# Optimization experiments

Measured on AMD Instinct MI355X. Metric: run time of the kernel, lower is better.

## Reference

```python
import jax, jax.numpy as jnp
import numpy as np

B, N, NUM_CLASSES = 2, 131072, 2
SCORE_THR, IOU_THR, OUT_NUM = 0.05, 0.7, 2000
NEG = -1e9  # sentinel for suppressed / below-threshold scores


def _decode(deltas, anchors):
    h = anchors[..., 2] - anchors[..., 0]
    w = anchors[..., 3] - anchors[..., 1]
    cy = (anchors[..., 2] + anchors[..., 0]) * 0.5
    cx = (anchors[..., 3] + anchors[..., 1]) * 0.5
    d = deltas * jnp.array([0.1, 0.1, 0.2, 0.2], dtype=deltas.dtype)
    cy = cy + d[..., 0] * h
    cx = cx + d[..., 1] * w
    h = h * jnp.exp(d[..., 2])
    w = w * jnp.exp(d[..., 3])
    return jnp.stack([cy - h * 0.5, cx - w * 0.5, cy + h * 0.5, cx + w * 0.5], axis=-1)


def _iou(box, boxes):
    # box [4] vs boxes [N,4] -> [N]
    y1 = jnp.maximum(box[0], boxes[:, 0])
    x1 = jnp.maximum(box[1], boxes[:, 1])
    y2 = jnp.minimum(box[2], boxes[:, 2])
    x2 = jnp.minimum(box[3], boxes[:, 3])
    inter = jnp.maximum(y2 - y1, 0.0) * jnp.maximum(x2 - x1, 0.0)
    a1 = (box[2] - box[0]) * (box[3] - box[1])
    a2 = (boxes[:, 2] - boxes[:, 0]) * (boxes[:, 3] - boxes[:, 1])
    return inter / (a1 + a2 - inter + 1e-8)


def _nms_single(boxes, scores, logits):
    # greedy NMS (= tf.image.non_max_suppression), then gather + pad_to_fixed_size
    live0 = jnp.where(scores > SCORE_THR, scores, NEG)

    def step(live, _):
        best = jnp.argmax(live)
        ok = live[best] > NEG * 0.5
        iou = _iou(boxes[best], boxes)
        live = jnp.where((iou > IOU_THR) & ok, NEG, live)
        live = live.at[best].set(NEG)
        return live, (best.astype(jnp.int32), ok.astype(boxes.dtype))

    _, (sel, valid) = jax.lax.scan(step, live0, None, length=OUT_NUM)
    vb = valid[:, None]  # [OUT_NUM,1] pad tag: 1 for real rows, 0 for padding
    out_boxes = boxes[sel] * vb
    out_scores = scores[sel][:, None] * vb
    out_logits = logits[sel] * vb
    return (jnp.concatenate([out_boxes, vb], axis=-1),
            jnp.concatenate([out_scores, vb], axis=-1),
            jnp.concatenate([out_logits, vb], axis=-1))


def _forward(deltas, class_logits, anchors):
    probs = jax.nn.softmax(class_logits, axis=-1)
    fg_scores = jnp.max(probs[..., 1:], axis=-1)  # [B,N]
    boxes = _decode(deltas, anchors)              # [B,N,4]
    return jax.vmap(_nms_single)(boxes, fg_scores, class_logits)


def setup_inputs() -> dict:
    key = jax.random.key(0)
    k1, k2, k3, k4, k5, k6 = jax.random.split(key, 6)
    deltas = jax.random.normal(k1, (B, N, 4), jnp.float32) * 0.5
    class_logits = jax.random.normal(k2, (B, N, NUM_CLASSES), jnp.float32)
    cy = jax.random.uniform(k3, (B, N), minval=0.0, maxval=800.0)
    cx = jax.random.uniform(k4, (B, N), minval=0.0, maxval=800.0)
    h = jax.random.uniform(k5, (B, N), minval=16.0, maxval=256.0)
    w = jax.random.uniform(k6, (B, N), minval=16.0, maxval=256.0)
    anchors = jnp.stack([cy - h * 0.5, cx - w * 0.5, cy + h * 0.5, cx + w * 0.5], axis=-1)
    return {"deltas": deltas, "class_logits": class_logits, "anchors": anchors}


def reference(deltas, class_logits, anchors):
    return _forward(deltas, class_logits, anchors)
```

## Files before the change

kernel.cpp:

```cpp
#include <hip/hip_runtime.h>
#include <stdint.h>
#include <stddef.h>

#define BATCH 2
#define NELEM 131072
#define OUT_NUM 2000
#define KCAP 32
#define PREWIN 16384
#define KPRE_W (PREWIN / 64)

__device__ __forceinline__ float exp32cr(float x) { return (float)exp((double)x); }

__device__ __forceinline__ bool iou_gt(float by1, float bx1, float by2, float bx2,
                                       float cy1, float cx1, float cy2, float cx2) {
    float y1 = fmaxf(by1, cy1), x1 = fmaxf(bx1, cx1);
    float y2 = fminf(by2, cy2), x2 = fminf(bx2, cx2);
    float ih = __fsub_rn(y2, y1), iw = __fsub_rn(x2, x1);
    if (ih <= 0.0f || iw <= 0.0f) return false;
    float inter = __fmul_rn(ih, iw);
    float a1 = __fmul_rn(__fsub_rn(by2, by1), __fsub_rn(bx2, bx1));
    float a2 = __fmul_rn(__fsub_rn(cy2, cy1), __fsub_rn(cx2, cx1));
    float den = __fadd_rn(__fsub_rn(__fadd_rn(a1, a2), inter), 1e-8f);
    float rhs = __fmul_rn(0.7f, den);
    if (inter > __fmul_rn(rhs, 1.0001f)) return true;
    if (inter < __fmul_rn(rhs, 0.9999f)) return false;
    return __fdiv_rn(inter, den) > 0.7f;
}
__device__ __forceinline__ bool iou_gt4(float4 a, float4 c) {
    return iou_gt(a.x, a.y, a.z, a.w, c.x, c.y, c.z, c.w);
}

__device__ __forceinline__ bool maybe4(float4 A, float4 C) {
    float dy = fabsf((A.x + A.z) - (C.x + C.z));
    float dx = fabsf((A.y + A.w) - (C.y + C.w));
    float hs = (A.z - A.x) + (C.z - C.x);
    float ws = (A.w - A.y) + (C.w - C.y);
    return (dy < 0.19f * hs) && (dx < 0.19f * ws);
}

__device__ __forceinline__ void decode_f(const float* __restrict__ deltas,
                                         const float* __restrict__ anchors,
                                         size_t gi, float* bx) {
    float a0 = anchors[4 * gi], a1 = anchors[4 * gi + 1];
    float a2 = anchors[4 * gi + 2], a3 = anchors[4 * gi + 3];
    float h = __fsub_rn(a2, a0), w = __fsub_rn(a3, a1);
    float cy = __fmul_rn(__fadd_rn(a2, a0), 0.5f);
    float cx = __fmul_rn(__fadd_rn(a3, a1), 0.5f);
    float d0 = __fmul_rn(deltas[4 * gi], 0.1f);
    float d1 = __fmul_rn(deltas[4 * gi + 1], 0.1f);
    float d2 = __fmul_rn(deltas[4 * gi + 2], 0.2f);
    float d3 = __fmul_rn(deltas[4 * gi + 3], 0.2f);
    cy = __fadd_rn(cy, __fmul_rn(d0, h));
    cx = __fadd_rn(cx, __fmul_rn(d1, w));
    h = __fmul_rn(h, exp32cr(d2));
    w = __fmul_rn(w, exp32cr(d3));
    bx[0] = __fsub_rn(cy, __fmul_rn(h, 0.5f));
    bx[1] = __fsub_rn(cx, __fmul_rn(w, 0.5f));
    bx[2] = __fadd_rn(cy, __fmul_rn(h, 0.5f));
    bx[3] = __fadd_rn(cx, __fmul_rn(w, 0.5f));
}

__device__ __forceinline__ float score_f(const float* __restrict__ logits, size_t gi) {
    float l0 = logits[2 * gi], l1 = logits[2 * gi + 1];
    float m = fmaxf(l0, l1);
    float e0 = exp32cr(__fsub_rn(l0, m));
    float e1 = exp32cr(__fsub_rn(l1, m));
    return __fdiv_rn(e1, __fadd_rn(e0, e1));
}

__global__ __launch_bounds__(256) void prep_kernel(
    const float* __restrict__ logits, uint64_t* __restrict__ keys,
    uint32_t* __restrict__ flag, uint32_t* __restrict__ state) {
    int i = blockIdx.x * 256 + threadIdx.x;
    if (i == 0) *flag = 0;
    if (i < 32) state[i] = 0;
    if (i >= BATCH * NELEM) return;
    float s = score_f(logits, (size_t)i);
    uint32_t idx = (uint32_t)(i & (NELEM - 1));
    uint64_t key = 0;
    if (s > 0.05f)
        key = ((uint64_t)__float_as_uint(s) << 17) | ((~idx) & 0x1FFFFu);
    keys[i] = key;
}

__global__ __launch_bounds__(1024) void bitonic_local_sort4(uint64_t* __restrict__ keys) {
    __shared__ uint64_t sh[4096];
    const int t = threadIdx.x;
    const size_t base = (size_t)blockIdx.x * 4096;
    for (int e = t; e < 4096; e += 1024) sh[e] = keys[base + e];
    __syncthreads();
    const int gb = (int)(base & (NELEM - 1));
    for (int k = 2; k <= 4096; k <<= 1) {
        for (int j = k >> 1; j >= 1; j >>= 1) {
            for (int pp = t; pp < 2048; pp += 1024) {
                int a = ((pp & ~(j - 1)) << 1) | (pp & (j - 1));
                bool ddd = (((gb + a) & k) == 0);
                uint64_t x = sh[a], y = sh[a + j];
                bool sw = ddd ? (x < y) : (x > y);
                if (sw) { sh[a] = y; sh[a + j] = x; }
            }
            __syncthreads();
        }
    }
    for (int e = t; e < 4096; e += 1024) keys[base + e] = sh[e];
}

__global__ __launch_bounds__(256) void bitonic_global_pass(uint64_t* __restrict__ keys,
                                                           int k, int j) {
    int tid = blockIdx.x * blockDim.x + threadIdx.x;
    const int half = NELEM / 2;
    int b = tid / half;
    int tt = tid - b * half;
    int a = ((tt & ~(j - 1)) << 1) | (tt & (j - 1));
    uint64_t* kb = keys + (size_t)b * NELEM;
    bool ddd = ((a & k) == 0);
    uint64_t x = kb[a], y = kb[a + j];
    bool sw = ddd ? (x < y) : (x > y);
    if (sw) { kb[a] = y; kb[a + j] = x; }
}

__global__ __launch_bounds__(256) void bitonic_global_fused2(uint64_t* __restrict__ keys,
                                                             int k, int j) {
    int tid = blockIdx.x * 256 + threadIdx.x;
    const int q = NELEM / 4;
    int b = tid / q;
    int tt = tid - b * q;
    int jh = j >> 1;
    int x = ((tt & ~(jh - 1)) << 2) | (tt & (jh - 1));
    uint64_t* kb = keys + (size_t)b * NELEM;
    bool ddd = ((x & k) == 0);
    uint64_t e0 = kb[x], e1 = kb[x + jh], e2 = kb[x + j], e3 = kb[x + j + jh];
    uint64_t tmp;
#define CMPEX(A, B) { bool sw = ddd ? (A < B) : (A > B); if (sw) { tmp = A; A = B; B = tmp; } }
    CMPEX(e0, e2) CMPEX(e1, e3)
    CMPEX(e0, e1) CMPEX(e2, e3)
#undef CMPEX
    kb[x] = e0; kb[x + jh] = e1; kb[x + j] = e2; kb[x + j + jh] = e3;
}

__global__ __launch_bounds__(1024) void bitonic_local_merge8(uint64_t* __restrict__ keys,
                                                             int k) {
    __shared__ uint64_t sh[8192];
    const int t = threadIdx.x;
    const size_t base = (size_t)blockIdx.x * 8192;
    for (int e = t; e < 8192; e += 1024) sh[e] = keys[base + e];
    __syncthreads();
    const bool ddd = (((int)(base & (NELEM - 1)) & k) == 0);
    for (int j = 4096; j >= 1; j >>= 1) {
        for (int pp = t; pp < 4096; pp += 1024) {
            int a = ((pp & ~(j - 1)) << 1) | (pp & (j - 1));
            uint64_t x = sh[a], y = sh[a + j];
            bool sw = ddd ? (x < y) : (x > y);
            if (sw) { sh[a] = y; sh[a + j] = x; }
        }
        __syncthreads();
    }
    for (int e = t; e < 8192; e += 1024) keys[base + e] = sh[e];
}

__global__ __launch_bounds__(256) void sort_check(const uint64_t* __restrict__ keys,
                                                  uint32_t* __restrict__ flag) {
    int i = blockIdx.x * 256 + threadIdx.x;
    if (i >= BATCH * NELEM) return;
    uint32_t q = (uint32_t)i & (NELEM - 1);
    if (q != NELEM - 1) {
        if (keys[i] < keys[i + 1]) atomicOr(flag, 1u);
    }
}

__global__ __launch_bounds__(256) void records_kernel(
    const uint64_t* __restrict__ keys, const float* __restrict__ deltas,
    const float* __restrict__ anchors, const float* __restrict__ logits,
    float* __restrict__ records, uint32_t* __restrict__ kcount, int M) {
    int g = blockIdx.x * 256 + threadIdx.x;
    if (g >= BATCH * M) return;
    kcount[g] = 0;
    int b = g / M, r = g - b * M;
    uint64_t key = keys[(size_t)b * NELEM + r];
    float4 r0, r1;
    if (key != 0) {
        uint32_t idx = (uint32_t)((~key) & 0x1FFFFu);
        size_t gi = (size_t)b * NELEM + idx;
        float bx[4];
        decode_f(deltas, anchors, gi, bx);
        r0 = make_float4(bx[0], bx[1], bx[2], bx[3]);
        r1 = make_float4(score_f(logits, gi), logits[2 * gi], logits[2 * gi + 1], 1.0f);
    } else {
        r0 = make_float4(0.f, 0.f, 0.f, 0.f);
        r1 = make_float4(0.f, 0.f, 0.f, 0.f);
    }
    float4* rp = (float4*)records;
    rp[(size_t)g * 2] = r0;
    rp[(size_t)g * 2 + 1] = r1;
}

__global__ __launch_bounds__(64) void mask_kernel(const float* __restrict__ records,
                                                  uint64_t* __restrict__ masks,
                                                  uint32_t* __restrict__ kcount,
                                                  uint16_t* __restrict__ klist, int M) {
    int ti = blockIdx.x, tj = blockIdx.y, b = blockIdx.z;
    if (tj > ti) return;
    int t = threadIdx.x;
    __shared__ float4 jb[64];
    __shared__ int jv[64];
    const float4* rp = (const float4*)records;
    {
        float4 rj  = rp[((size_t)b * M + (size_t)tj * 64 + t) * 2];
        float4 rj1 = rp[((size_t)b * M + (size_t)tj * 64 + t) * 2 + 1];
        jb[t] = rj;
        jv[t] = (rj1.w != 0.f);
    }
    const int i = ti * 64 + t;
    float4 ri  = rp[((size_t)b * M + i) * 2];
    float4 ri1 = rp[((size_t)b * M + i) * 2 + 1];
    bool iv = (ri1.w != 0.f);
    __syncthreads();
    uint64_t word = 0;
    if (iv) {
        for (int jj = 0; jj < 64; ++jj) {
            bool earlier = (tj < ti) || (jj < t);
            if (earlier && jv[jj] && maybe4(jb[jj], ri) && iou_gt4(jb[jj], ri)) {
                word |= 1ull << jj;
                uint32_t slot = atomicAdd(&kcount[(size_t)b * M + i], 1u);
                if (slot < KCAP)
                    klist[((size_t)b * M + i) * KCAP + slot] = (uint16_t)(tj * 64 + jj);
            }
        }
    }
    masks[((size_t)b * M + i) * (size_t)(M >> 6) + tj] = word;
}

__global__ void nms_walk(
    const float* __restrict__ records, const uint64_t* __restrict__ masks,
    const uint32_t* __restrict__ kcount, const uint16_t* __restrict__ klist,
    float4* __restrict__ accbox, uint32_t* __restrict__ state,
    float* __restrict__ out, int M) {
    const int b = blockIdx.x;
    const int t = threadIdx.x;
    const int Wm = M >> 6;
    const int NC = M >> 8;
    const uint64_t* mb = masks + (size_t)b * M * (size_t)Wm;
    const float4* rp = (const float4*)records + (size_t)b * M * 2;

    __shared__ uint64_t accset[128];
    __shared__ uint64_t bwLDS[256][4];
    __shared__ uint8_t kf[256];
    __shared__ float4 recLDS[512];
    __shared__ uint32_t s_state[16];

    for (int w = t; w < 128; w += blockDim.x) accset[w] = 0;
    __syncthreads();

    int n_acc = 0, done = 0;
    for (int ci = 0; ci < NC && !done; ++ci) {
        const int p = ci << 8;
        const int pw = ci << 2;
        if (t < 256) {
            const int gi = p + t;
            uint32_t cnt = kcount[(size_t)b * M + gi];
            uint64_t rq0 = 0, rq1 = 0, rq2 = 0, rq3 = 0;
            bool kill = false;
            if (cnt <= KCAP) {
                const uint16_t* lp = klist + ((size_t)b * M + gi) * KCAP;
                for (uint32_t u = 0; u < cnt; ++u) {
                    int j = lp[u];
                    if (j < p) {
                        if ((accset[j >> 6] >> (j & 63)) & 1) kill = true;
                    } else {
                        int d = j - p;
                        uint64_t bit = 1ull << (d & 63);
                        switch (d >> 6) {
                            case 0: rq0 |= bit; break;
                            case 1: rq1 |= bit; break;
                            case 2: rq2 |= bit; break;
                            default: rq3 |= bit; break;
                        }
                    }
                }
            } else {
                const uint64_t* row = mb + (size_t)gi * Wm;
                uint64_t o = 0;
                for (int w = 0; w < pw; ++w) o |= row[w] & accset[w];
                kill = (o != 0);
                rq0 = row[pw]; rq1 = row[pw + 1];
                rq2 = row[pw + 2]; rq3 = row[pw + 3];
            }
            kf[t] = kill ? 1 : 0;
            bwLDS[t][0] = rq0; bwLDS[t][1] = rq1;
            bwLDS[t][2] = rq2; bwLDS[t][3] = rq3;
        } else if (t < 512) {
            int i0 = t - 256;
            recLDS[i0] = rp[(size_t)p * 2 + i0];
            recLDS[i0 + 256] = rp[(size_t)p * 2 + i0 + 256];
        }
        __syncthreads();

        if (t < 64) {
            const int l = t;
            uint64_t b00 = bwLDS[l][0], b01 = bwLDS[l][1], b02 = bwLDS[l][2], b03 = bwLDS[l][3];
            uint64_t b10 = bwLDS[64 + l][0], b11 = bwLDS[64 + l][1], b12 = bwLDS[64 + l][2], b13 = bwLDS[64 + l][3];
            uint64_t b20 = bwLDS[128 + l][0], b21 = bwLDS[128 + l][1], b22 = bwLDS[128 + l][2], b23 = bwLDS[128 + l][3];
            uint64_t b30 = bwLDS[192 + l][0], b31 = bwLDS[192 + l][1], b32 = bwLDS[192 + l][2], b33 = bwLDS[192 + l][3];
            uint64_t vm0 = __ballot(recLDS[2 * l + 1].w != 0.f);
            uint64_t vm1 = __ballot(recLDS[2 * (64 + l) + 1].w != 0.f);
            uint64_t vm2 = __ballot(recLDS[2 * (128 + l) + 1].w != 0.f);
            uint64_t vm3 = __ballot(recLDS[2 * (192 + l) + 1].w != 0.f);
            uint64_t k0 = __ballot(kf[l] != 0);
            uint64_t k1 = __ballot(kf[64 + l] != 0);
            uint64_t k2 = __ballot(kf[128 + l] != 0);
            uint64_t k3 = __ballot(kf[192 + l] != 0);
            uint64_t e0m = __ballot((b00 | b01 | b02 | b03) == 0);
            uint64_t e1m = __ballot((b10 | b11 | b12 | b13) == 0);
            uint64_t e2m = __ballot((b20 | b21 | b22 | b23) == 0);
            uint64_t e3m = __ballot((b30 | b31 | b32 | b33) == 0);
            if (t == 0) {
                uint64_t t0 = vm0 & ~k0, t1 = vm1 & ~k1, t2 = vm2 & ~k2, t3 = vm3 & ~k3;
                uint64_t a0 = t0 & e0m, a1 = t1 & e1m, a2 = t2 & e2m, a3 = t3 & e3m;
                uint64_t c0 = t0 & ~e0m, c1 = t1 & ~e1m, c2 = t2 & ~e2m, c3 = t3 & ~e3m;
#define RESOLVE(cq, aq, base) \
    while (cq) { int cb = __builtin_ctzll(cq); cq &= cq - 1; \
        int idx = (base) + cb; \
        uint64_t w0 = bwLDS[idx][0], w1 = bwLDS[idx][1]; \
        uint64_t w2 = bwLDS[idx][2], w3 = bwLDS[idx][3]; \
        if (!((w0 & a0) | (w1 & a1) | (w2 & a2) | (w3 & a3))) aq |= (1ull << cb); }
                RESOLVE(c0, a0, 0)
                RESOLVE(c1, a1, 64)
                RESOLVE(c2, a2, 128)
                RESOLVE(c3, a3, 192)
#undef RESOLVE
                int n = n_acc;
                int dn = ((vm0 & vm1 & vm2 & vm3) != ~0ull) ? 1 : 0;
                int tot = (int)(__popcll(a0) + __popcll(a1) + __popcll(a2) + __popcll(a3));
                int rem = OUT_NUM - n;
                if (tot >= rem) {
                    int keep = rem;
#define TRUNC(w) { int pc = (int)__popcll(w); \
    if (keep >= pc) keep -= pc; \
    else { while ((int)__popcll(w) > keep) w &= ~(1ull << (63 - __builtin_clzll(w))); keep = 0; } }
                    TRUNC(a0) TRUNC(a1) TRUNC(a2) TRUNC(a3)
#undef TRUNC
                    n = OUT_NUM; dn = 1;
                } else {
                    n += tot;
                }
                s_state[0] = (uint32_t)n_acc;
                s_state[1] = (uint32_t)n;
                s_state[2] = (uint32_t)dn;
                s_state[3] = (uint32_t)a0; s_state[4] = (uint32_t)(a0 >> 32);
                s_state[5] = (uint32_t)a1; s_state[6] = (uint32_t)(a1 >> 32);
                s_state[7] = (uint32_t)a2; s_state[8] = (uint32_t)(a2 >> 32);
                s_state[9] = (uint32_t)a3; s_state[10] = (uint32_t)(a3 >> 32);
                accset[pw] = a0; accset[pw + 1] = a1;
                accset[pw + 2] = a2; accset[pw + 3] = a3;
            }
        }
        __syncthreads();
        int r0 = (int)s_state[0];
        n_acc = (int)s_state[1];
        done = (int)s_state[2];
        uint64_t amA = ((uint64_t)s_state[4] << 32) | s_state[3];
        uint64_t amB = ((uint64_t)s_state[6] << 32) | s_state[5];
        uint64_t amC = ((uint64_t)s_state[8] << 32) | s_state[7];
        uint64_t amD = ((uint64_t)s_state[10] << 32) | s_state[9];

        if (t < 256) {
            int q = t >> 6, ll = t & 63;
            uint64_t amq = q == 0 ? amA : q == 1 ? amB : q == 2 ? amC : amD;
            if ((amq >> ll) & 1) {
                int base = r0;
                if (q > 0) base += (int)__popcll(amA);
                if (q > 1) base += (int)__popcll(amB);
                if (q > 2) base += (int)__popcll(amC);
                int row = base + (int)__popcll(amq & ((1ull << ll) - 1ull));
                float4 cb = recLDS[t * 2], cm = recLDS[t * 2 + 1];
                accbox[(size_t)b * OUT_NUM + row] = cb;
                float* ob = out + ((size_t)b * OUT_NUM + row) * 5;
                ob[0] = cb.x; ob[1] = cb.y; ob[2] = cb.z; ob[3] = cb.w; ob[4] = 1.0f;
                float* os = out + (size_t)BATCH * OUT_NUM * 5 +
                            ((size_t)b * OUT_NUM + row) * 2;
                os[0] = cm.x; os[1] = 1.0f;
                float* ol = out + (size_t)BATCH * OUT_NUM * 7 +
                            ((size_t)b * OUT_NUM + row) * 3;
                ol[0] = cm.y; ol[1] = cm.z; ol[2] = 1.0f;
            }
        }
        __syncthreads();
    }
    if (t == 0) {
        state[b * 16] = (uint32_t)n_acc;
        state[b * 16 + 1] = (uint32_t)done;
    }
}

__global__ __launch_bounds__(1024) void prekill_kernel(
    const uint64_t* __restrict__ keys, const float* __restrict__ deltas,
    const float* __restrict__ anchors, const float4* __restrict__ accbox,
    const uint32_t* __restrict__ state, uint64_t* __restrict__ kpre, int Mend) {
    const int blk = blockIdx.x, b = blockIdx.y;
    const int t = threadIdx.x;
    const int c = t & 63, g = t >> 6;
    const int n1 = (int)state[b * 16];
    __shared__ float4 aF[OUT_NUM];
    __shared__ float4 jb[64];
    __shared__ uint8_t kfl[64];
    for (int r = t; r < n1; r += 1024) aF[r] = accbox[(size_t)b * OUT_NUM + r];
    if (t < 64) {
        kfl[t] = 0;
        int j = Mend + blk * 64 + t;
        uint64_t key = keys[(size_t)b * NELEM + j];
        float4 bx4 = make_float4(0.f, 0.f, 0.f, 0.f);
        if (key != 0) {
            uint32_t idx = (uint32_t)((~key) & 0x1FFFFu);
            size_t gi = (size_t)b * NELEM + idx;
            float bx[4];
            decode_f(deltas, anchors, gi, bx);
            bx4 = make_float4(bx[0], bx[1], bx[2], bx[3]);
        }
        jb[t] = bx4;
    }
    __syncthreads();
    float4 cb = jb[c];
    float csy = cb.x + cb.z, csx = cb.y + cb.w;
    float ch19 = 0.19f * (cb.z - cb.x), cw19 = 0.19f * (cb.w - cb.y);
    bool k = false;
    for (int a = g; a < n1; a += 16) {
        float4 af = aF[a];
        float asy = af.x + af.z, asx = af.y + af.w;
        float ah19 = 0.19f * (af.z - af.x), aw19 = 0.19f * (af.w - af.y);
        if (fabsf(asy - csy) < ah19 + ch19 && fabsf(asx - csx) < aw19 + cw19) {
            if (iou_gt4(af, cb)) { k = true; break; }
        }
    }
    if (k) kfl[c] = 1;
    __syncthreads();
    if (t < 64) {
        uint64_t w = __ballot(kfl[t] != 0);
        if (t == 0) kpre[(size_t)b * KPRE_W + blk] = w;
    }
}

__global__ __launch_bounds__(512) void nms_tail(
    const uint64_t* __restrict__ keys, const float* __restrict__ deltas,
    const float* __restrict__ logits, const float* __restrict__ anchors,
    const float4* __restrict__ accbox, const uint32_t* __restrict__ state,
    const uint64_t* __restrict__ kpre, float* __restrict__ out,
    int Mend, int hasPre) {
    const int b = blockIdx.x;
    const int t = threadIdx.x;
    const int l = t & 63;

    __shared__ float4 aF4[OUT_NUM];
    __shared__ float4 aS4[OUT_NUM];
    __shared__ float4 cbox[256], cmeta[256];
    __shared__ uint32_t transW[256][8];
    __shared__ uint8_t kf2[512];
    __shared__ uint64_t kpreLDS[4];
    __shared__ uint32_t s_state[16];

    if (t == 0) {
        s_state[0] = state[b * 16];
        s_state[1] = state[b * 16 + 1];
    }
    __syncthreads();
    int n_acc = (int)s_state[0];
    int done = (int)s_state[1];
    const int tailStart = n_acc;
    for (int r = t; r < n_acc; r += 512) {
        float4 ab = accbox[(size_t)b * OUT_NUM + r];
        aF4[r] = ab;
        aS4[r] = make_float4(ab.x + ab.z, ab.y + ab.w, ab.z - ab.x, ab.w - ab.y);
    }
    __syncthreads();

    for (int p = Mend; p < NELEM && !done; p += 256) {
        const bool inwin = hasPre && (p < Mend + PREWIN);
        for (int i = t; i < 2048; i += 512) ((uint32_t*)transW)[i] = 0;
        if (t < 256) {
            uint64_t key = keys[(size_t)b * NELEM + p + t];
            float4 bx4 = make_float4(0.f, 0.f, 0.f, 0.f);
            float4 mt = make_float4(0.f, 0.f, 0.f, 0.f);
            if (key != 0) {
                uint32_t idx = (uint32_t)((~key) & 0x1FFFFu);
                size_t gi = (size_t)b * NELEM + idx;
                float bx[4];
                decode_f(deltas, anchors, gi, bx);
                bx4 = make_float4(bx[0], bx[1], bx[2], bx[3]);
                mt = make_float4(score_f(logits, gi), logits[2 * gi],
                                 logits[2 * gi + 1], 1.0f);
            }
            cbox[t] = bx4; cmeta[t] = mt;
        }
        if (t < 4)
            kpreLDS[t] = inwin ? kpre[(size_t)b * KPRE_W + ((p - Mend) >> 6) + t] : 0ull;
        __syncthreads();

        {
            const int c = t & 255, g = t >> 8;
            float4 cb = cbox[c];
            bool pkc = inwin && ((kpreLDS[c >> 6] >> (c & 63)) & 1);
            bool valid = (cmeta[c].w != 0.f) && !pkc;
            float csy = cb.x + cb.z, csx = cb.y + cb.w;
            float chh = cb.z - cb.x, cww = cb.w - cb.y;
            bool k = false;
            int aStart = inwin ? tailStart : 0;
            if (valid) {
                for (int a = aStart + g; a < n_acc; a += 2) {
                    float4 as = aS4[a];
                    if (fabsf(as.x - csy) < 0.19f * (as.z + chh) &&
                        fabsf(as.y - csx) < 0.19f * (as.w + cww)) {
                        if (iou_gt4(aF4[a], cb)) { k = true; break; }
                    }
                }
            }
            kf2[t] = k ? 1 : 0;
        }
        __syncthreads();

        for (int pid = t; pid < 256 * 256; pid += 512) {
            int c0 = pid >> 8, c1 = pid & 255;
            if (c1 > c0 && cmeta[c0].w != 0.f && cmeta[c1].w != 0.f) {
                bool d0 = (inwin && ((kpreLDS[c0 >> 6] >> (c0 & 63)) & 1)) ||
                          kf2[c0] || kf2[256 + c0];
                bool d1 = (inwin && ((kpreLDS[c1 >> 6] >> (c1 & 63)) & 1)) ||
                          kf2[c1] || kf2[256 + c1];
                if (!d0 && !d1 && maybe4(cbox[c0], cbox[c1]) &&
                    iou_gt4(cbox[c0], cbox[c1]))
                    atomicOr(&transW[c1][c0 >> 5], 1u << (c0 & 31));
            }
        }
        __syncthreads();

        if (t < 64) {
            uint64_t bw00, bw01, bw02, bw03, bw10, bw11, bw12, bw13;
            uint64_t bw20, bw21, bw22, bw23, bw30, bw31, bw32, bw33;
            bw00 = ((uint64_t)transW[l][1] << 32) | transW[l][0];
            bw01 = ((uint64_t)transW[l][3] << 32) | transW[l][2];
            bw02 = ((uint64_t)transW[l][5] << 32) | transW[l][4];
            bw03 = ((uint64_t)transW[l][7] << 32) | transW[l][6];
            bw10 = ((uint64_t)transW[64 + l][1] << 32) | transW[64 + l][0];
            bw11 = ((uint64_t)transW[64 + l][3] << 32) | transW[64 + l][2];
            bw12 = ((uint64_t)transW[64 + l][5] << 32) | transW[64 + l][4];
            bw13 = ((uint64_t)transW[64 + l][7] << 32) | transW[64 + l][6];
            bw20 = ((uint64_t)transW[128 + l][1] << 32) | transW[128 + l][0];
            bw21 = ((uint64_t)transW[128 + l][3] << 32) | transW[128 + l][2];
            bw22 = ((uint64_t)transW[128 + l][5] << 32) | transW[128 + l][4];
            bw23 = ((uint64_t)transW[128 + l][7] << 32) | transW[128 + l][6];
            bw30 = ((uint64_t)transW[192 + l][1] << 32) | transW[192 + l][0];
            bw31 = ((uint64_t)transW[192 + l][3] << 32) | transW[192 + l][2];
            bw32 = ((uint64_t)transW[192 + l][5] << 32) | transW[192 + l][4];
            bw33 = ((uint64_t)transW[192 + l][7] << 32) | transW[192 + l][6];
            uint64_t vm0 = __ballot(cmeta[l].w != 0.f);
            uint64_t vm1 = __ballot(cmeta[64 + l].w != 0.f);
            uint64_t vm2 = __ballot(cmeta[128 + l].w != 0.f);
            uint64_t vm3 = __ballot(cmeta[192 + l].w != 0.f);
            uint64_t k0 = kpreLDS[0] | __ballot((kf2[l] | kf2[256 + l]) != 0);
            uint64_t k1 = kpreLDS[1] | __ballot((kf2[64 + l] | kf2[320 + l]) != 0);
            uint64_t k2 = kpreLDS[2] | __ballot((kf2[128 + l] | kf2[384 + l]) != 0);
            uint64_t k3 = kpreLDS[3] | __ballot((kf2[192 + l] | kf2[448 + l]) != 0);
            uint64_t t0 = vm0 & ~k0, t1 = vm1 & ~k1, t2 = vm2 & ~k2, t3 = vm3 & ~k3;
            uint64_t am0 = 0, am1 = 0, am2 = 0, am3 = 0;
            int n = n_acc;
            int dn = ((vm0 & vm1 & vm2 & vm3) != ~0ull);
            while (t0 | t1 | t2 | t3) {
                int qb; uint64_t w;
                if (t0)      { qb = 0; w = t0; }
                else if (t1) { qb = 1; w = t1; }
                else if (t2) { qb = 2; w = t2; }
                else         { qb = 3; w = t3; }
                int lb = __builtin_ctzll(w);
                uint64_t bit = 1ull << lb;
                if (qb == 0) { am0 |= bit; t0 &= ~bit; }
                else if (qb == 1) { am1 |= bit; t1 &= ~bit; }
                else if (qb == 2) { am2 |= bit; t2 &= ~bit; }
                else { am3 |= bit; t3 &= ~bit; }
                ++n;
                if (n == OUT_NUM) { dn = 1; break; }
                uint64_t s0 = qb == 0 ? bw00 : qb == 1 ? bw01 : qb == 2 ? bw02 : bw03;
                uint64_t s1 = qb == 0 ? bw10 : qb == 1 ? bw11 : qb == 2 ? bw12 : bw13;
                uint64_t s2 = qb == 0 ? bw20 : qb == 1 ? bw21 : qb == 2 ? bw22 : bw23;
                uint64_t s3 = qb == 0 ? bw30 : qb == 1 ? bw31 : qb == 2 ? bw32 : bw33;
                t0 &= ~__ballot(((s0 >> lb) & 1) != 0);
                t1 &= ~__ballot(((s1 >> lb) & 1) != 0);
                t2 &= ~__ballot(((s2 >> lb) & 1) != 0);
                t3 &= ~__ballot(((s3 >> lb) & 1) != 0);
            }
            if (t == 0) {
                s_state[0] = (uint32_t)n_acc;
                s_state[1] = (uint32_t)n;
                s_state[2] = (uint32_t)dn;
                s_state[3] = (uint32_t)am0; s_state[4] = (uint32_t)(am0 >> 32);
                s_state[5] = (uint32_t)am1; s_state[6] = (uint32_t)(am1 >> 32);
                s_state[7] = (uint32_t)am2; s_state[8] = (uint32_t)(am2 >> 32);
                s_state[9] = (uint32_t)am3; s_state[10] = (uint32_t)(am3 >> 32);
            }
        }
        __syncthreads();
        int r0 = (int)s_state[0];
        n_acc = (int)s_state[1];
        done = (int)s_state[2];
        uint64_t amA = ((uint64_t)s_state[4] << 32) | s_state[3];
        uint64_t amB = ((uint64_t)s_state[6] << 32) | s_state[5];
        uint64_t amC = ((uint64_t)s_state[8] << 32) | s_state[7];
        uint64_t amD = ((uint64_t)s_state[10] << 32) | s_state[9];

        if (t < 256) {
            int q = t >> 6, ll = t & 63;
            uint64_t amq = q == 0 ? amA : q == 1 ? amB : q == 2 ? amC : amD;
            if ((amq >> ll) & 1) {
                int base = r0;
                if (q > 0) base += (int)__popcll(amA);
                if (q > 1) base += (int)__popcll(amB);
                if (q > 2) base += (int)__popcll(amC);
                int row = base + (int)__popcll(amq & ((1ull << ll) - 1ull));
                float4 cb = cbox[t];
                float4 cm = cmeta[t];
                aF4[row] = cb;
                aS4[row] = make_float4(cb.x + cb.z, cb.y + cb.w,
                                       cb.z - cb.x, cb.w - cb.y);
                float* ob = out + ((size_t)b * OUT_NUM + row) * 5;
                ob[0] = cb.x; ob[1] = cb.y; ob[2] = cb.z; ob[3] = cb.w; ob[4] = 1.0f;
                float* os = out + (size_t)BATCH * OUT_NUM * 5 +
                            ((size_t)b * OUT_NUM + row) * 2;
                os[0] = cm.x; os[1] = 1.0f;
                float* ol = out + (size_t)BATCH * OUT_NUM * 7 +
                            ((size_t)b * OUT_NUM + row) * 3;
                ol[0] = cm.y; ol[1] = cm.z; ol[2] = 1.0f;
            }
        }
        __syncthreads();
    }

    for (int r = n_acc + t; r < OUT_NUM; r += 512) {
        float* ob = out + ((size_t)b * OUT_NUM + r) * 5;
        ob[0] = 0.f; ob[1] = 0.f; ob[2] = 0.f; ob[3] = 0.f; ob[4] = 0.f;
        float* os = out + (size_t)BATCH * OUT_NUM * 5 + ((size_t)b * OUT_NUM + r) * 2;
        os[0] = 0.f; os[1] = 0.f;
        float* ol = out + (size_t)BATCH * OUT_NUM * 7 + ((size_t)b * OUT_NUM + r) * 3;
        ol[0] = 0.f; ol[1] = 0.f; ol[2] = 0.f;
    }
    if (t == 0 && n_acc < OUT_NUM) out[0] = 2.0e5f;
}

__global__ void canary_kernel(const uint32_t* __restrict__ flag, float* __restrict__ out,
                              int code) {
    if (code) { out[0] = 3.0e5f; return; }
    if (*flag) out[0] = 1.0e5f;
}

extern "C" void kernel_launch(void* const* d_in, const int* in_sizes, int n_in,
                              void* d_out, int out_size, void* d_ws, size_t ws_size,
                              hipStream_t stream) {
    const float* deltas  = (const float*)d_in[0];
    const float* logits  = (const float*)d_in[1];
    const float* anchors = (const float*)d_in[2];
    float* out = (float*)d_out;

    const size_t keysB = (size_t)BATCH * NELEM * 8;
    const size_t flagOff = keysB;
    const size_t stateOff = keysB + 256;
    const size_t kpreOff = keysB + 512;
    const size_t accOff = kpreOff + 8192;
    const size_t recOff = accOff + 65536;
    if (ws_size < recOff) {
        canary_kernel<<<1, 1, 0, stream>>>((const uint32_t*)d_ws, out, 1);
        return;
    }
    int M = 0, wbs = 512;
    const int tiers[3] = {8192, 4096, 2048};
    const int twbs[3]  = {512, 576, 640};
    for (int i = 0; i < 3; ++i) {
        int cand = tiers[i];
        size_t need = recOff + (size_t)BATCH * cand * 32 +
                      (size_t)BATCH * cand * (cand / 8) +
                      (size_t)BATCH * cand * 4 +
                      (size_t)BATCH * cand * KCAP * 2;
        if (ws_size >= need) { M = cand; wbs = twbs[i]; break; }
    }

    uint64_t* keys = (uint64_t*)d_ws;
    uint32_t* flag = (uint32_t*)((char*)d_ws + flagOff);
    uint32_t* state = (uint32_t*)((char*)d_ws + stateOff);
    uint64_t* kpre = (uint64_t*)((char*)d_ws + kpreOff);
    float4* accbox = (float4*)((char*)d_ws + accOff);
    float* records = (float*)((char*)d_ws + recOff);
    uint64_t* masks = (uint64_t*)((char*)d_ws + recOff + (size_t)BATCH * M * 32);
    uint32_t* kcount = (uint32_t*)((char*)masks + (size_t)BATCH * M * (M / 8));
    uint16_t* klist = (uint16_t*)((char*)kcount + (size_t)BATCH * M * 4);

    prep_kernel<<<(BATCH * NELEM) / 256, 256, 0, stream>>>(logits, keys, flag, state);

    bitonic_local_sort4<<<BATCH * NELEM / 4096, 1024, 0, stream>>>(keys);
    bitonic_local_merge8<<<BATCH * NELEM / 8192, 1024, 0, stream>>>(keys, 8192);
    bitonic_global_pass<<<(BATCH * NELEM / 2) / 256, 256, 0, stream>>>(keys, 16384, 8192);
    bitonic_local_merge8<<<BATCH * NELEM / 8192, 1024, 0, stream>>>(keys, 16384);
    bitonic_global_fused2<<<(BATCH * NELEM / 4) / 256, 256, 0, stream>>>(keys, 32768, 16384);
    bitonic_local_merge8<<<BATCH * NELEM / 8192, 1024, 0, stream>>>(keys, 32768);
    bitonic_global_fused2<<<(BATCH * NELEM / 4) / 256, 256, 0, stream>>>(keys, 65536, 32768);
    bitonic_global_pass<<<(BATCH * NELEM / 2) / 256, 256, 0, stream>>>(keys, 65536, 8192);
    bitonic_local_merge8<<<BATCH * NELEM / 8192, 1024, 0, stream>>>(keys, 65536);
    bitonic_global_fused2<<<(BATCH * NELEM / 4) / 256, 256, 0, stream>>>(keys, 131072, 65536);
    bitonic_global_fused2<<<(BATCH * NELEM / 4) / 256, 256, 0, stream>>>(keys, 131072, 16384);
    bitonic_local_merge8<<<BATCH * NELEM / 8192, 1024, 0, stream>>>(keys, 131072);

    sort_check<<<(BATCH * NELEM) / 256, 256, 0, stream>>>(keys, flag);
    if (M > 0) {
        records_kernel<<<(BATCH * M) / 256, 256, 0, stream>>>(keys, deltas, anchors,
                                                              logits, records, kcount, M);
        dim3 mg(M / 64, M / 64, BATCH);
        mask_kernel<<<mg, 64, 0, stream>>>(records, masks, kcount, klist, M);
        nms_walk<<<BATCH, wbs, 0, stream>>>(records, masks, kcount, klist,
                                            accbox, state, out, M);
        dim3 pg(PREWIN / 64, BATCH);
        prekill_kernel<<<pg, 1024, 0, stream>>>(keys, deltas, anchors, accbox, state,
                                                kpre, M);
    }
    nms_tail<<<BATCH, 512, 0, stream>>>(keys, deltas, logits, anchors, accbox, state,
                                        kpre, out, M, (M > 0) ? 1 : 0);
    canary_kernel<<<1, 1, 0, stream>>>(flag, out, 0);
}
```

Measured before the change: 282.4 us.

## Fuse bitonic global stages into 3- and 4-level kernels; early-exit prekill loop

Adds bitonic kernels that do three and four consecutive compare-exchange levels per thread on 8 or 16 elements held in registers. These replace the pairs of fused2/global_pass launches in the large merge stages, which cuts global memory round trips and kernel launches. The prekill loop also polls a shared kill flag so threads can stop once another thread has marked the candidate. The cost is higher register pressure, with 16 uint64 values per thread in fused4, and strided access patterns.

Measured after the change: 293.7 us. +4.0%, slower.

```diff
diff --git a/kernel.cpp b/kernel.cpp
--- a/kernel.cpp
+++ b/kernel.cpp
@@ -136,6 +136,59 @@
     CMPEX(e0, e1) CMPEX(e2, e3)
 #undef CMPEX
     kb[x] = e0; kb[x + jh] = e1; kb[x + j] = e2; kb[x + j + jh] = e3;
+}
+
+__global__ __launch_bounds__(256) void bitonic_global_fused3(uint64_t* __restrict__ keys,
+                                                             int k, int j) {
+    int tid = blockIdx.x * 256 + threadIdx.x;
+    const int q = NELEM / 8;
+    int b = tid / q;
+    int tt = tid - b * q;
+    int jq = j >> 2;
+    int x = ((tt & ~(jq - 1)) << 3) | (tt & (jq - 1));
+    uint64_t* kb = keys + (size_t)b * NELEM;
+    bool ddd = ((x & k) == 0);
+    uint64_t e0 = kb[x], e1 = kb[x + jq], e2 = kb[x + 2 * jq], e3 = kb[x + 3 * jq];
+    uint64_t e4 = kb[x + 4 * jq], e5 = kb[x + 5 * jq], e6 = kb[x + 6 * jq], e7 = kb[x + 7 * jq];
+    uint64_t tmp;
+#define CMPEX(A, B) { bool sw = ddd ? (A < B) : (A > B); if (sw) { tmp = A; A = B; B = tmp; } }
+    CMPEX(e0, e4) CMPEX(e1, e5) CMPEX(e2, e6) CMPEX(e3, e7)
+    CMPEX(e0, e2) CMPEX(e1, e3) CMPEX(e4, e6) CMPEX(e5, e7)
+    CMPEX(e0, e1) CMPEX(e2, e3) CMPEX(e4, e5) CMPEX(e6, e7)
+#undef CMPEX
+    kb[x] = e0; kb[x + jq] = e1; kb[x + 2 * jq] = e2; kb[x + 3 * jq] = e3;
+    kb[x + 4 * jq] = e4; kb[x + 5 * jq] = e5; kb[x + 6 * jq] = e6; kb[x + 7 * jq] = e7;
+}
+
+__global__ __launch_bounds__(256) void bitonic_global_fused4(uint64_t* __restrict__ keys,
+                                                             int k, int j) {
+    int tid = blockIdx.x * 256 + threadIdx.x;
+    const int q = NELEM / 16;
+    int b = tid / q;
+    int tt = tid - b * q;
+    int jq = j >> 3;
+    int x = ((tt & ~(jq - 1)) << 4) | (tt & (jq - 1));
+    uint64_t* kb = keys + (size_t)b * NELEM;
+    bool ddd = ((x & k) == 0);
+    uint64_t e[16];
+#pragma unroll
+    for (int i = 0; i < 16; ++i) e[i] = kb[x + i * jq];
+    uint64_t tmp;
+#define CMPEX(A, B) { bool sw = ddd ? (e[A] < e[B]) : (e[A] > e[B]); \
+    if (sw) { tmp = e[A]; e[A] = e[B]; e[B] = tmp; } }
+#pragma unroll
+    for (int i = 0; i < 8; ++i) CMPEX(i, i + 8)
+#pragma unroll
+    for (int g2 = 0; g2 < 16; g2 += 8) {
+        CMPEX(g2 + 0, g2 + 4) CMPEX(g2 + 1, g2 + 5) CMPEX(g2 + 2, g2 + 6) CMPEX(g2 + 3, g2 + 7)
+    }
+#pragma unroll
+    for (int g2 = 0; g2 < 16; g2 += 4) { CMPEX(g2 + 0, g2 + 2) CMPEX(g2 + 1, g2 + 3) }
+#pragma unroll
+    for (int g2 = 0; g2 < 16; g2 += 2) CMPEX(g2, g2 + 1)
+#undef CMPEX
+#pragma unroll
+    for (int i = 0; i < 16; ++i) kb[x + i * jq] = e[i];
 }
 
 __global__ __launch_bounds__(1024) void bitonic_local_merge8(uint64_t* __restrict__ keys,
@@ -419,11 +472,13 @@
         jb[t] = bx4;
     }
     __syncthreads();
+    volatile uint8_t* vk = kfl;
     float4 cb = jb[c];
     float csy = cb.x + cb.z, csx = cb.y + cb.w;
     float ch19 = 0.19f * (cb.z - cb.x), cw19 = 0.19f * (cb.w - cb.y);
     bool k = false;
     for (int a = g; a < n1; a += 16) {
+        if (vk[c]) break;
         float4 af = aF[a];
         float asy = af.x + af.z, asx = af.y + af.w;
         float ah19 = 0.19f * (af.z - af.x), aw19 = 0.19f * (af.w - af.y);
@@ -695,11 +750,9 @@
     bitonic_local_merge8<<<BATCH * NELEM / 8192, 1024, 0, stream>>>(keys, 16384);
     bitonic_global_fused2<<<(BATCH * NELEM / 4) / 256, 256, 0, stream>>>(keys, 32768, 16384);
     bitonic_local_merge8<<<BATCH * NELEM / 8192, 1024, 0, stream>>>(keys, 32768);
-    bitonic_global_fused2<<<(BATCH * NELEM / 4) / 256, 256, 0, stream>>>(keys, 65536, 32768);
-    bitonic_global_pass<<<(BATCH * NELEM / 2) / 256, 256, 0, stream>>>(keys, 65536, 8192);
+    bitonic_global_fused3<<<(BATCH * NELEM / 8) / 256, 256, 0, stream>>>(keys, 65536, 32768);
     bitonic_local_merge8<<<BATCH * NELEM / 8192, 1024, 0, stream>>>(keys, 65536);
-    bitonic_global_fused2<<<(BATCH * NELEM / 4) / 256, 256, 0, stream>>>(keys, 131072, 65536);
-    bitonic_global_fused2<<<(BATCH * NELEM / 4) / 256, 256, 0, stream>>>(keys, 131072, 16384);
+    bitonic_global_fused4<<<(BATCH * NELEM / 16) / 256, 256, 0, stream>>>(keys, 131072, 65536);
     bitonic_local_merge8<<<BATCH * NELEM / 8192, 1024, 0, stream>>>(keys, 131072);
 
     sort_check<<<(BATCH * NELEM) / 256, 256, 0, stream>>>(keys, flag);
```
